# Performance work log

Hardware: AMD Instinct MI355X
Metric: run time of the kernel (lower is better)

Reference implementation:

```python
import jax, jax.numpy as jnp
import numpy as np

H = 2048
MAX_DEPTH = 2
BASIS = 4


def setup_inputs() -> dict:
    key = jax.random.key(0)
    ks = jax.random.split(key, 16)
    s = 0.02

    def w(k, shape):
        return jax.random.normal(k, shape, dtype=jnp.float32) * s

    return dict(
        x=jax.random.normal(ks[0], (1, H), dtype=jnp.float32),
        h=jax.random.normal(ks[1], (1, H), dtype=jnp.float32),
        c=jax.random.normal(ks[2], (1, H), dtype=jnp.float32),
        Wq=w(ks[3], (H, H)), Wk=w(ks[4], (H, H)), Wv=w(ks[5], (H, H)), Wo=w(ks[6], (H, H)),
        Wih=w(ks[7], (H, 4 * H)), Whh=w(ks[8], (H, 4 * H)),
        b_lstm=jnp.zeros((4 * H,), jnp.float32),
        router_w=w(ks[9], (H, BASIS)), router_b=jnp.zeros((BASIS,), jnp.float32),
        expert_w=w(ks[10], (BASIS, H, H)), expert_b=jnp.zeros((BASIS, H), jnp.float32),
        dr_w=w(ks[11], (H, MAX_DEPTH + 1)),
        # bias the depth router toward the deepest choice so the recursion tree is exercised
        dr_b=jnp.array([0.0, 1.0, 5.0], jnp.float32),
        ram_w=w(ks[12], (2 * H, H)), ram_b=jnp.zeros((H,), jnp.float32),
        ag_w=w(ks[13], (2 * H, H)), ag_b=jnp.zeros((H,), jnp.float32),
    )


def reference(x, h, c, Wq, Wk, Wv, Wo, Wih, Whh, b_lstm, router_w, router_b,
              expert_w, expert_b, dr_w, dr_b, ram_w, ram_b, ag_w, ag_b):
    def cell_step(x_, h_, c_):
        # Single-token multi-head attention: softmax over a length-1 axis is
        # identically 1, so attention collapses to (h @ Wv) @ Wo; Wq/Wk are
        # parameters with zero effective gradient (matches torch behavior).
        attn = (h_ @ Wv) @ Wo
        gates = x_ @ Wih + attn @ Whh + b_lstm  # [1, 4H]
        i, f, g, o = jnp.split(gates, 4, axis=1)
        c2 = jax.nn.sigmoid(f) * c_ + jax.nn.sigmoid(i) * jnp.tanh(g)
        h2 = jax.nn.sigmoid(o) * jnp.tanh(c2)
        return h2, h2, c2

    def path_gate(hh):
        p = jax.nn.softmax(hh @ router_w + router_b, axis=1)          # [1, E]
        eo = jnp.einsum('bh,ehk->bek', hh, expert_w) + expert_b        # [1, E, H]
        return jnp.einsum('be,bek->bk', p, eo)                         # [1, H]

    def ramanujan(states):
        # alternating-harmonic (Ramanujan-summation style) weighted reduction
        agg = states[0] * 0.0
        for n, s in enumerate(states):
            agg = agg + (((-1.0) ** n) / (n + 1)) * s
        return jnp.concatenate([agg, states[0]], axis=1) @ ram_w + ram_b

    def fwd(x_, h_, c_, depth):
        so, hs, cs = cell_step(x_, h_, c_)
        hp = path_gate(hs)
        # mirrors torch.no_grad() + .item() host sync
        chosen = int(jnp.argmax(hp @ dr_w + dr_b, axis=1)[0])
        steps = min(chosen, max(0, MAX_DEPTH - depth))
        if steps <= 0:
            return so, hp, cs
        h_cur, c_cur, final = hp, cs, so
        states = [h_cur]
        for _ in range(steps):
            damping = 1.0 / (depth + 1) ** 2
            ro, hnr, cn = fwd(x_, h_cur, c_cur, depth + 1)
            h_next = h_cur + damping * (hnr - h_cur)  # torch.lerp
            states.append(h_next)
            h_cur, c_cur, final = h_next, cn, ro
        anchor = ramanujan(states)
        g = jax.nn.sigmoid(jnp.concatenate([h_cur, anchor], axis=1) @ ag_w + ag_b)
        return final, g * anchor + (1.0 - g) * h_cur, c_cur

    return fwd(x, h, c, 0)
```

## Files before the change

kernel.cpp:

```cpp
#include <hip/hip_runtime.h>
#include <math.h>


#define H 2048
#define NB 512
#define PREP_NB 2048
typedef unsigned short u16;
typedef float f4v __attribute__((ext_vector_type(4)));

struct P {
  const float *x, *h0, *c0, *Wv, *Wo, *Wih, *Whh, *b_lstm, *router_w, *router_b,
              *expert_w, *expert_b, *dr_w, *dr_b, *ram_w, *ram_b, *ag_w, *ag_b;
  const u16 *bWv, *bWo, *bWhh, *bEx, *bRam, *bAg;
  u16 *mWv, *mWo, *mWhh, *mEx, *mRam, *mAg;
  float* out;
  float* ws;
};

constexpr int CTRU   = 16384;
constexpr int DL     = 16384;
constexpr int GT     = 16400;
constexpr int NODE   = 24592;
constexpr int NODESZ = 26624;
constexpr int THV = 0, ATT = 2048, GAC = 4096, EO = 12288, SO = 20480, CS = 22528, HP = 24576;
constexpr int FIN    = NODE + 5 * NODESZ;
constexpr int FINSZ  = 8192;
constexpr int ANC = 0, GCC = 2048, HNo = 4096, AGGo = 6144;
constexpr int RH1 = FIN + 3 * FINSZ;
constexpr int RF1 = RH1 + 2048;
constexpr int RC1 = RH1 + 4096;
constexpr int ZTOT = 5 * 20480 + 3 * 4096;
constexpr size_t BF_BYTE_OFF = 786432;
constexpr size_t oWo  = 4194304;
constexpr size_t oWhh = 8388608;
constexpr size_t oEx  = 25165824;
constexpr size_t oRam = 41943040;
constexpr size_t oAg  = 50331648;
constexpr size_t BF_NODE = 41943040;
constexpr size_t BF_ALL  = 58720256;

__device__ __forceinline__ float sigm(float v) { return 1.f / (1.f + expf(-v)); }

__device__ __forceinline__ float coh_f(const float* p) {
  return __hip_atomic_load(p, __ATOMIC_RELAXED, __HIP_MEMORY_SCOPE_AGENT);
}
__device__ __forceinline__ void coh_st(float* p, float v) {
  __hip_atomic_store(p, v, __ATOMIC_RELAXED, __HIP_MEMORY_SCOPE_AGENT);
}

__device__ __forceinline__ float bfl(unsigned u) { union { unsigned x; float f; } c; c.x = u << 16; return c.f; }
__device__ __forceinline__ float bfh(unsigned u) { union { unsigned x; float f; } c; c.x = u & 0xFFFF0000u; return c.f; }
__device__ __forceinline__ u16 f2bf(float f) {
  unsigned u = __float_as_uint(f);
  u += 0x7FFFu + ((u >> 16) & 1u);
  return (u16)(u >> 16);
}
__device__ __forceinline__ unsigned pk2(float a, float b) {
  return (unsigned)f2bf(a) | ((unsigned)f2bf(b) << 16);
}

template <typename WT> struct W4;
template <> struct W4<float> {
  static __device__ __forceinline__ void load(const float* p, float* w) {
    const float4 v = *reinterpret_cast<const float4*>(p);
    w[0] = v.x; w[1] = v.y; w[2] = v.z; w[3] = v.w;
  }
};
template <> struct W4<u16> {
  static __device__ __forceinline__ void load(const u16* p, float* w) {
    const uint2 u = *reinterpret_cast<const uint2*>(p);
    w[0] = bfl(u.x); w[1] = bfh(u.x); w[2] = bfl(u.y); w[3] = bfh(u.y);
  }
};

template <typename WT> __device__ __forceinline__ const WT* selWv(const P& p);
template <> __device__ __forceinline__ const float* selWv<float>(const P& p) { return p.Wv; }
template <> __device__ __forceinline__ const u16*   selWv<u16>(const P& p)   { return p.bWv; }
template <typename WT> __device__ __forceinline__ const WT* selWo(const P& p);
template <> __device__ __forceinline__ const float* selWo<float>(const P& p) { return p.Wo; }
template <> __device__ __forceinline__ const u16*   selWo<u16>(const P& p)   { return p.bWo; }
template <typename WT> __device__ __forceinline__ const WT* selWhh(const P& p);
template <> __device__ __forceinline__ const float* selWhh<float>(const P& p) { return p.Whh; }
template <> __device__ __forceinline__ const u16*   selWhh<u16>(const P& p)   { return p.bWhh; }
template <typename WT> __device__ __forceinline__ const WT* selEx(const P& p);
template <> __device__ __forceinline__ const float* selEx<float>(const P& p) { return p.expert_w; }
template <> __device__ __forceinline__ const u16*   selEx<u16>(const P& p)   { return p.bEx; }
template <typename WT> __device__ __forceinline__ const WT* selRam(const P& p);
template <> __device__ __forceinline__ const float* selRam<float>(const P& p) { return p.ram_w; }
template <> __device__ __forceinline__ const u16*   selRam<u16>(const P& p)   { return p.bRam; }
template <typename WT> __device__ __forceinline__ const WT* selAg(const P& p);
template <> __device__ __forceinline__ const float* selAg<float>(const P& p) { return p.ag_w; }
template <> __device__ __forceinline__ const u16*   selAg<u16>(const P& p)   { return p.bAg; }

__device__ __forceinline__ int dsteps(const float* dla, const float* drb, int mx) {
  const float l0 = coh_f(dla + 0) + drb[0];
  const float l1 = coh_f(dla + 1) + drb[1];
  const float l2 = coh_f(dla + 2) + drb[2];
  int ch = 0; float bv = l0;
  if (l1 > bv) { bv = l1; ch = 1; }
  if (l2 > bv) { bv = l2; ch = 2; }
  return ch < mx ? ch : mx;
}

__device__ __forceinline__ bool pred(const float* ws, const float* drb, int code) {
  if (code == 0) return true;
  const int s0 = dsteps(ws + DL, drb, 2);
  switch (code) {
    case 1: return s0 >= 1;
    case 2: return s0 >= 1 && dsteps(ws + DL + 4, drb, 1) >= 1;
    case 3: return s0 >= 2;
    case 4: return s0 >= 2 && dsteps(ws + DL + 8, drb, 1) >= 1;
  }
  return true;
}

__device__ __forceinline__ void resbar(unsigned* ctr, int phase) {
  asm volatile("s_waitcnt vmcnt(0)" ::: "memory");
  __syncthreads();
  __shared__ int lastB;
  if (threadIdx.x == 0) {
    lastB = 0;
    unsigned* line = ctr + (blockIdx.x & 31) * 16;
    const unsigned prev = __hip_atomic_fetch_add(line, 1u, __ATOMIC_RELAXED, __HIP_MEMORY_SCOPE_AGENT);
    if (prev == (unsigned)(16 * phase) - 1u) {
      const unsigned m = __hip_atomic_fetch_add(ctr + 512, 1u, __ATOMIC_RELAXED, __HIP_MEMORY_SCOPE_AGENT);
      if (m == (unsigned)(32 * phase) - 1u) lastB = 1;
    }
  }
  __syncthreads();
  if (lastB) {
    if (threadIdx.x < 32)
      __hip_atomic_store(ctr + (40 + threadIdx.x) * 16, (unsigned)phase,
                         __ATOMIC_RELAXED, __HIP_MEMORY_SCOPE_AGENT);
  } else if (threadIdx.x == 0) {
    const unsigned* rel = ctr + (40 + (blockIdx.x & 31)) * 16;
    long t = 0;
    while (__hip_atomic_load(rel, __ATOMIC_RELAXED, __HIP_MEMORY_SCOPE_AGENT) < (unsigned)phase) {
      __builtin_amdgcn_s_sleep(2);
      if (++t > 30000000L) break;
    }
  }
  __syncthreads();
}

template <int CHUNK, int XMODE, typename WT, int CONV, int TPB>
__device__ __forceinline__ void gemv_phase(
    int bid, int G,
    const float* xA, const float* xB, int splitPt, const float* xBias,
    const WT* __restrict__ W, float* __restrict__ y, int N,
    u16* convDst, float* shx, float4* red)
{
  constexpr int NSUB = TPB / 64;
  constexpr int LEN  = CHUNK / NSUB;
  const int tid = threadIdx.x, lane = tid & 63, tsub = tid >> 6;
  const int g = bid % G, s = bid / G;
  const int base = s * CHUNK;
  for (int idx = tid; idx < CHUNK; idx += TPB) {
    const int i = base + idx;
    float v;
    if (XMODE == 0)      v = (i < splitPt) ? coh_f(xA + i) : coh_f(xB + (i - splitPt));
    else if (XMODE == 1) v = coh_f(xA + i);
    else                 v = (i < splitPt) ? coh_f(xA + i)
                                           : (xBias[i - splitPt] + coh_f(xB + (i - splitPt)));
    shx[idx] = v;
  }
  __syncthreads();
  const int j = (g << 8) + (lane << 2);
  const WT* Wp = W + (size_t)(base + tsub * LEN) * N + j;
  float ax = 0.f, ay = 0.f, az = 0.f, aw = 0.f;
#pragma unroll
  for (int t = 0; t < LEN; ++t) {
    const float xi = shx[tsub * LEN + t];
    float w[4];
    if constexpr (CONV) {
      const f4v a = __builtin_nontemporal_load(
          reinterpret_cast<const f4v*>(reinterpret_cast<const float*>(Wp) + (size_t)t * N));
      w[0] = a.x; w[1] = a.y; w[2] = a.z; w[3] = a.w;
      uint2 o; o.x = pk2(w[0], w[1]); o.y = pk2(w[2], w[3]);
      *reinterpret_cast<uint2*>(convDst + (size_t)(base + tsub * LEN + t) * N + j) = o;
    } else {
      W4<WT>::load(Wp + (size_t)t * N, w);
    }
    ax = fmaf(xi, w[0], ax); ay = fmaf(xi, w[1], ay);
    az = fmaf(xi, w[2], az); aw = fmaf(xi, w[3], aw);
  }
  red[tid] = make_float4(ax, ay, az, aw);
  __syncthreads();
  if (tsub == 0) {
    float4 a = red[tid];
#pragma unroll
    for (int q = 1; q < NSUB; ++q) {
      const float4 b = red[tid + q * 64];
      a.x += b.x; a.y += b.y; a.z += b.z; a.w += b.w;
    }
    atomicAdd(&y[j + 0], a.x);
    atomicAdd(&y[j + 1], a.y);
    atomicAdd(&y[j + 2], a.z);
    atomicAdd(&y[j + 3], a.w);
  }
}

template <typename WT, int CONV>
__device__ void expert_phase(const P& p, float* nb, const float* c_in, const float* gt,
                             u16* convDst, float* shx, float4* red)
{
  const int tid = threadIdx.x, lane = tid & 63, w = tid >> 6;
  const int g = blockIdx.x & 31, s = blockIdx.x >> 5;
  const int i0 = s * 128;
  if (tid < 128) {
    const int i = i0 + tid;
    const float gi = p.b_lstm[i]         + coh_f(gt + i)         + coh_f(nb + GAC + i);
    const float gf = p.b_lstm[H + i]     + coh_f(gt + H + i)     + coh_f(nb + GAC + H + i);
    const float gg = p.b_lstm[2 * H + i] + coh_f(gt + 2 * H + i) + coh_f(nb + GAC + 2 * H + i);
    const float go = p.b_lstm[3 * H + i] + coh_f(gt + 3 * H + i) + coh_f(nb + GAC + 3 * H + i);
    const float c2 = sigm(gf) * coh_f(c_in + i) + sigm(gi) * tanhf(gg);
    const float h2 = sigm(go) * tanhf(c2);
    shx[tid] = h2;
    if (g == 0) { coh_st(nb + SO + i, h2); coh_st(nb + CS + i, c2); }
  }
  __syncthreads();
  const int j = (g << 8) + (lane << 2);
  const int e = j >> 11, k = j & (H - 1);
  const size_t tileOff = ((size_t)e << 22) + (size_t)(i0 + w * 16) * H + k;
  const WT* Wp = selEx<WT>(p) + tileOff;
  float ax = 0.f, ay = 0.f, az = 0.f, aw = 0.f;
#pragma unroll
  for (int t = 0; t < 16; ++t) {
    const float xi = shx[w * 16 + t];
    float wv[4];
    if constexpr (CONV) {
      const f4v a = __builtin_nontemporal_load(
          reinterpret_cast<const f4v*>(reinterpret_cast<const float*>(Wp) + (size_t)t * H));
      wv[0] = a.x; wv[1] = a.y; wv[2] = a.z; wv[3] = a.w;
      uint2 o; o.x = pk2(wv[0], wv[1]); o.y = pk2(wv[2], wv[3]);
      *reinterpret_cast<uint2*>(convDst + tileOff + (size_t)t * H) = o;
    } else {
      W4<WT>::load(Wp + (size_t)t * H, wv);
    }
    ax = fmaf(xi, wv[0], ax); ay = fmaf(xi, wv[1], ay);
    az = fmaf(xi, wv[2], az); aw = fmaf(xi, wv[3], aw);
  }
  red[tid] = make_float4(ax, ay, az, aw);
  __syncthreads();
  if (w == 0) {
    float4 a = red[tid];
#pragma unroll
    for (int q = 1; q < 8; ++q) {
      const float4 b = red[tid + q * 64];
      a.x += b.x; a.y += b.y; a.z += b.z; a.w += b.w;
    }
    atomicAdd(&nb[EO + j + 0], a.x);
    atomicAdd(&nb[EO + j + 1], a.y);
    atomicAdd(&nb[EO + j + 2], a.z);
    atomicAdd(&nb[EO + j + 3], a.w);
  }
}

template <typename WT, int CONV>
__device__ __forceinline__ void node_body(const P& p, float* nb,
                                          const float* hv, const float* cv,
                                          unsigned* ctr, int& ph,
                                          float* shx, float4* red)
{
  gemv_phase<32, 1, WT, CONV, 512>(blockIdx.x, 8, hv, nullptr, 0, nullptr,
                                   selWv<WT>(p), nb + THV, H, p.mWv, shx, red);
  resbar(ctr, ++ph);
  gemv_phase<32, 1, WT, CONV, 512>(blockIdx.x, 8, nb + THV, nullptr, 0, nullptr,
                                   selWo<WT>(p), nb + ATT, H, p.mWo, shx, red);
  resbar(ctr, ++ph);
  gemv_phase<128, 1, WT, CONV, 512>(blockIdx.x, 32, nb + ATT, nullptr, 0, nullptr,
                                    selWhh<WT>(p), nb + GAC, 4 * H, p.mWhh, shx, red);
  resbar(ctr, ++ph);
  expert_phase<WT, CONV>(p, nb, cv, p.ws + GT, p.mEx, shx, red);
  resbar(ctr, ++ph);
}

template <typename WT, int CONV>
__device__ __forceinline__ void fin_body(const P& p, float* fb,
                                         const float* aggv, const float* phpv, const float* hnv,
                                         unsigned* ctr, int& ph,
                                         float* shx, float4* red)
{
  gemv_phase<64, 0, WT, CONV, 512>(blockIdx.x, 8, aggv, phpv, H, nullptr,
                                   selRam<WT>(p), fb + ANC, H, p.mRam, shx, red);
  resbar(ctr, ++ph);
  gemv_phase<64, 2, WT, CONV, 512>(blockIdx.x, 8, hnv, fb + ANC, H, p.ram_b,
                                   selAg<WT>(p), fb + GCC, H, p.mAg, shx, red);
  resbar(ctr, ++ph);
}

__device__ void combine_phase(const P& p, float* nb, float* dla, int leaf, float damping,
                              const float* php, float* hn, float* agg, float4* red)
{
  const int tid = threadIdx.x;
  float r0 = 0.f, r1 = 0.f, r2 = 0.f, r3 = 0.f;
  for (int i = tid; i < H; i += 512) {
    const float hh = coh_f(nb + SO + i);
    const float4 rw = *reinterpret_cast<const float4*>(p.router_w + i * 4);
    r0 = fmaf(hh, rw.x, r0); r1 = fmaf(hh, rw.y, r1);
    r2 = fmaf(hh, rw.z, r2); r3 = fmaf(hh, rw.w, r3);
  }
  red[tid] = make_float4(r0, r1, r2, r3);
  __syncthreads();
  for (int off = 256; off > 0; off >>= 1) {
    if (tid < off) {
      const float4 b = red[tid + off];
      red[tid].x += b.x; red[tid].y += b.y; red[tid].z += b.z; red[tid].w += b.w;
    }
    __syncthreads();
  }
  const float4 L = red[0];
  __syncthreads();
  const float l0 = L.x + p.router_b[0], l1 = L.y + p.router_b[1];
  const float l2 = L.z + p.router_b[2], l3 = L.w + p.router_b[3];
  const float m = fmaxf(fmaxf(l0, l1), fmaxf(l2, l3));
  const float e0 = expf(l0 - m), e1 = expf(l1 - m), e2 = expf(l2 - m), e3 = expf(l3 - m);
  const float inv = 1.f / (e0 + e1 + e2 + e3);
  const float q0 = e0 * inv, q1 = e1 * inv, q2 = e2 * inv, q3 = e3 * inv;
  const int jj = blockIdx.x * 256 + (tid & 255);
  float v = 0.f;
  if (tid < 256) {
    v = q0 * (p.expert_b[jj]         + coh_f(nb + EO + jj))
      + q1 * (p.expert_b[H + jj]     + coh_f(nb + EO + H + jj))
      + q2 * (p.expert_b[2 * H + jj] + coh_f(nb + EO + 2 * H + jj))
      + q3 * (p.expert_b[3 * H + jj] + coh_f(nb + EO + 3 * H + jj));
  }
  if (leaf) {
    if (tid < 256) {
      const float h0v = coh_f(php + jj);
      const float hnv = h0v + damping * (v - h0v);
      coh_st(hn + jj, hnv);
      coh_st(agg + jj, h0v - 0.5f * hnv);
    }
  } else {
    if (tid < 256) coh_st(nb + HP + jj, v);
    red[tid] = (tid < 256)
        ? make_float4(v * p.dr_w[jj * 3 + 0], v * p.dr_w[jj * 3 + 1], v * p.dr_w[jj * 3 + 2], 0.f)
        : make_float4(0.f, 0.f, 0.f, 0.f);
    __syncthreads();
    for (int off = 256; off > 0; off >>= 1) {
      if (tid < off) {
        const float4 b = red[tid + off];
        red[tid].x += b.x; red[tid].y += b.y; red[tid].z += b.z;
      }
      __syncthreads();
    }
    if (tid == 0) {
      atomicAdd(&dla[0], red[0].x);
      atomicAdd(&dla[1], red[0].y);
      atomicAdd(&dla[2], red[0].z);
    }
  }
}

__device__ void tail_fsel(const P& p, float* ws) {
  if (threadIdx.x >= 256) return;
  if (dsteps(ws + DL, p.dr_b, 2) < 1) return;
  const bool deep = dsteps(ws + DL + 4, p.dr_b, 1) >= 1;
  const int jj = blockIdx.x * 256 + threadIdx.x;
  const float* n1 = ws + NODE + 1 * NODESZ;
  const float* n2 = ws + NODE + 2 * NODESZ;
  const float* fb = ws + FIN;
  float rh, rf, rc;
  if (deep) {
    const float gacc = p.ag_b[jj] + coh_f(fb + GCC + jj);
    const float anc  = p.ram_b[jj] + coh_f(fb + ANC + jj);
    const float g = sigm(gacc);
    rh = g * anc + (1.f - g) * coh_f(fb + HNo + jj);
    rf = coh_f(n2 + SO + jj); rc = coh_f(n2 + CS + jj);
  } else {
    rh = coh_f(n1 + HP + jj); rf = coh_f(n1 + SO + jj); rc = coh_f(n1 + CS + jj);
  }
  coh_st(ws + RH1 + jj, rh); coh_st(ws + RF1 + jj, rf); coh_st(ws + RC1 + jj, rc);
}

__device__ void tail1(const P& p, float* ws) {
  if (threadIdx.x >= 256) return;
  const int s0 = dsteps(ws + DL, p.dr_b, 2);
  if (s0 < 1) return;
  const int jj = blockIdx.x * 256 + threadIdx.x;
  const float* n0 = ws + NODE;
  const float* n3 = ws + NODE + 3 * NODESZ;
  const float* n4 = ws + NODE + 4 * NODESZ;
  const float* fb3 = ws + FIN + FINSZ;
  float* fb0 = ws + FIN + 2 * FINSZ;
  const float r1 = coh_f(ws + RH1 + jj);
  float rh3 = 0.f, rf3 = 0.f, rc3 = 0.f;
  if (s0 >= 2) {
    if (dsteps(ws + DL + 8, p.dr_b, 1) >= 1) {
      const float gacc = p.ag_b[jj] + coh_f(fb3 + GCC + jj);
      const float anc  = p.ram_b[jj] + coh_f(fb3 + ANC + jj);
      const float g = sigm(gacc);
      rh3 = g * anc + (1.f - g) * coh_f(fb3 + HNo + jj);
      rf3 = coh_f(n4 + SO + jj); rc3 = coh_f(n4 + CS + jj);
    } else {
      rh3 = coh_f(n3 + HP + jj); rf3 = coh_f(n3 + SO + jj); rc3 = coh_f(n3 + CS + jj);
    }
  }
  float ag = coh_f(n0 + HP + jj) - 0.5f * r1;
  float hc, oF, oC;
  if (s0 >= 2) { ag += (1.f / 3.f) * rh3; hc = rh3; oF = rf3; oC = rc3; }
  else { hc = r1; oF = coh_f(ws + RF1 + jj); oC = coh_f(ws + RC1 + jj); }
  coh_st(fb0 + AGGo + jj, ag); coh_st(fb0 + HNo + jj, hc);
  p.out[jj] = oF; p.out[2 * H + jj] = oC;
}

__device__ void tail2(const P& p, float* ws) {
  if (threadIdx.x >= 256) return;
  const int s0 = dsteps(ws + DL, p.dr_b, 2);
  const int jj = blockIdx.x * 256 + threadIdx.x;
  const float* n0 = ws + NODE;
  const float* fb0 = ws + FIN + 2 * FINSZ;
  if (s0 == 0) {
    p.out[jj] = coh_f(n0 + SO + jj);
    p.out[H + jj] = coh_f(n0 + HP + jj);
    p.out[2 * H + jj] = coh_f(n0 + CS + jj);
  } else {
    const float gacc = p.ag_b[jj] + coh_f(fb0 + GCC + jj);
    const float anc  = p.ram_b[jj] + coh_f(fb0 + ANC + jj);
    const float g = sigm(gacc);
    p.out[H + jj] = g * anc + (1.f - g) * coh_f(fb0 + HNo + jj);
  }
}

__global__ void __launch_bounds__(256) k_zero(P p) {
  float* ws = p.ws;
  const int gtid = blockIdx.x * 256 + threadIdx.x;
  const int gsz = gridDim.x * 256;
  unsigned* u = (unsigned*)ws;
  for (int i = gtid; i < CTRU; i += gsz) u[i] = 0u;
  if (gtid < 12) ws[DL + gtid] = 0.f;
  for (int i = gtid; i < 8192; i += gsz) ws[GT + i] = 0.f;
}

__global__ void __launch_bounds__(256) k_prep(P p) {
  float* ws = p.ws;
  __shared__ float shx[128];
  __shared__ float4 red[256];
  const size_t gtid = (size_t)blockIdx.x * 256 + threadIdx.x;
  const size_t nthr = (size_t)PREP_NB * 256;
  for (size_t i = gtid; i < (size_t)ZTOT; i += nthr) {
    if (i < 5 * 20480) {
      const int n = (int)(i / 20480), off = (int)(i % 20480);
      ws[NODE + n * NODESZ + off] = 0.f;
    } else {
      const int j = (int)(i - 5 * 20480);
      ws[FIN + (j >> 12) * FINSZ + (j & 4095)] = 0.f;
    }
  }
  gemv_phase<32, 0, float, 0, 256>(blockIdx.x, 32, p.x, p.x, 1 << 30, nullptr,
                                   p.Wih, ws + GT, 4 * H, nullptr, shx, red);
}

template <typename WT, int CONV>
__global__ void __launch_bounds__(512, 2) k_node(
    P p, int nodeIdx, int ctrIdx, int predCode,
    const float* hv, const float* cv, float* dla)
{
  float* ws = p.ws;
  if (!pred(ws, p.dr_b, predCode)) return;
  __shared__ float shx[128];
  __shared__ float4 red[512];
  float* nb = ws + NODE + nodeIdx * NODESZ;
  unsigned* ctr = (unsigned*)ws + ctrIdx * 2048;
  int ph = 0;
  node_body<WT, CONV>(p, nb, hv, cv, ctr, ph, shx, red);
  if (blockIdx.x >= 8) return;
  combine_phase(p, nb, dla, 0, 0.f, nullptr, nullptr, nullptr, red);
}

template <typename WT, typename WTF, int CONVF>
__global__ void __launch_bounds__(512, 2) k_n2fin(P p) {
  float* ws = p.ws;
  if (!pred(ws, p.dr_b, 1)) return;
  __shared__ float shx[128];
  __shared__ float4 red[512];
  float* nb  = ws + NODE + 2 * NODESZ;
  float* n1  = ws + NODE + 1 * NODESZ;
  float* fb1 = ws + FIN;
  unsigned* ctr = (unsigned*)ws + 2 * 2048;
  int ph = 0;
  if (pred(ws, p.dr_b, 2)) {
    node_body<WT, 0>(p, nb, n1 + HP, n1 + CS, ctr, ph, shx, red);
    if (blockIdx.x < 8)
      combine_phase(p, nb, nullptr, 1, 0.25f, n1 + HP, fb1 + HNo, fb1 + AGGo, red);
    resbar(ctr, ++ph);
  }
  fin_body<WTF, CONVF>(p, fb1, fb1 + AGGo, n1 + HP, fb1 + HNo, ctr, ph, shx, red);
  if (blockIdx.x < 8) tail_fsel(p, ws);
}

template <typename WT, typename WTF>
__global__ void __launch_bounds__(512, 2) k_n4fin(P p) {
  float* ws = p.ws;
  __shared__ float shx[128];
  __shared__ float4 red[512];
  float* nb  = ws + NODE + 4 * NODESZ;
  float* n3  = ws + NODE + 3 * NODESZ;
  float* n0  = ws + NODE;
  float* fb3 = ws + FIN + FINSZ;
  float* fb0 = ws + FIN + 2 * FINSZ;
  unsigned* ctr = (unsigned*)ws + 5 * 2048;
  int ph = 0;
  const int s0v = dsteps(ws + DL, p.dr_b, 2);
  if (s0v >= 2 && dsteps(ws + DL + 8, p.dr_b, 1) >= 1) {
    node_body<WT, 0>(p, nb, n3 + HP, n3 + CS, ctr, ph, shx, red);
    if (blockIdx.x < 8)
      combine_phase(p, nb, nullptr, 1, 0.25f, n3 + HP, fb3 + HNo, fb3 + AGGo, red);
    resbar(ctr, ++ph);
    fin_body<WTF, 0>(p, fb3, fb3 + AGGo, n3 + HP, fb3 + HNo, ctr, ph, shx, red);
  }
  if (s0v >= 1) {
    if (blockIdx.x < 8) tail1(p, ws);
    resbar(ctr, ++ph);
    fin_body<WTF, 0>(p, fb0, fb0 + AGGo, n0 + HP, fb0 + HNo, ctr, ph, shx, red);
  }
  if (blockIdx.x < 8) tail2(p, ws);
}

extern "C" void kernel_launch(void* const* d_in, const int* in_sizes, int n_in,
                              void* d_out, int out_size, void* d_ws, size_t ws_size,
                              hipStream_t stream) {
  P p;
  p.x = (const float*)d_in[0];  p.h0 = (const float*)d_in[1];  p.c0 = (const float*)d_in[2];
  p.Wv = (const float*)d_in[5]; p.Wo = (const float*)d_in[6];
  p.Wih = (const float*)d_in[7]; p.Whh = (const float*)d_in[8];
  p.b_lstm = (const float*)d_in[9];
  p.router_w = (const float*)d_in[10]; p.router_b = (const float*)d_in[11];
  p.expert_w = (const float*)d_in[12]; p.expert_b = (const float*)d_in[13];
  p.dr_w = (const float*)d_in[14]; p.dr_b = (const float*)d_in[15];
  p.ram_w = (const float*)d_in[16]; p.ram_b = (const float*)d_in[17];
  p.ag_w = (const float*)d_in[18]; p.ag_b = (const float*)d_in[19];
  p.out = (float*)d_out;
  p.ws = (float*)d_ws;

  const bool useBf    = ws_size >= BF_BYTE_OFF + BF_NODE * 2 + 1024;
  const bool useBfFin = ws_size >= BF_BYTE_OFF + BF_ALL * 2 + 1024;
  u16* bf = (u16*)((char*)d_ws + BF_BYTE_OFF);
  p.bWv = bf;        p.bWo = bf + oWo;   p.bWhh = bf + oWhh;
  p.bEx = bf + oEx;  p.bRam = bf + oRam; p.bAg  = bf + oAg;
  p.mWv = bf;        p.mWo = bf + oWo;   p.mWhh = bf + oWhh;
  p.mEx = bf + oEx;  p.mRam = bf + oRam; p.mAg  = bf + oAg;

  float* ws = p.ws;
  auto nb = [&](int n) { return ws + NODE + n * NODESZ; };

  k_zero<<<16, 256, 0, stream>>>(p);
  k_prep<<<PREP_NB, 256, 0, stream>>>(p);

  if (useBf)
    k_node<float, 1><<<NB, 512, 0, stream>>>(p, 0, 0, 0, p.h0, p.c0, ws + DL);
  else
    k_node<float, 0><<<NB, 512, 0, stream>>>(p, 0, 0, 0, p.h0, p.c0, ws + DL);

  if (useBf)
    k_node<u16, 0><<<NB, 512, 0, stream>>>(p, 1, 1, 1, nb(0) + HP, nb(0) + CS, ws + DL + 4);
  else
    k_node<float, 0><<<NB, 512, 0, stream>>>(p, 1, 1, 1, nb(0) + HP, nb(0) + CS, ws + DL + 4);

  if (useBf && useBfFin)
    k_n2fin<u16, float, 1><<<NB, 512, 0, stream>>>(p);
  else if (useBf)
    k_n2fin<u16, float, 0><<<NB, 512, 0, stream>>>(p);
  else
    k_n2fin<float, float, 0><<<NB, 512, 0, stream>>>(p);

  if (useBf)
    k_node<u16, 0><<<NB, 512, 0, stream>>>(p, 3, 4, 3, ws + RH1, ws + RC1, ws + DL + 8);
  else
    k_node<float, 0><<<NB, 512, 0, stream>>>(p, 3, 4, 3, ws + RH1, ws + RC1, ws + DL + 8);

  if (useBf && useBfFin)
    k_n4fin<u16, u16><<<NB, 512, 0, stream>>>(p);
  else if (useBf)
    k_n4fin<u16, float><<<NB, 512, 0, stream>>>(p);
  else
    k_n4fin<float, float><<<NB, 512, 0, stream>>>(p);
}
```

Measured before the change: 337.6 us.

## Merge node kernels into fewer persistent launches with grid barriers

The seven launches are cut to four. The prep work is folded into k_zero and into the first node kernel, where the x@Wih GEMV runs before a grid barrier. Node 1 is fused with node 2 and fin, and node 3 with node 4 and fin, using resbar barriers between phases. This removes per-launch overhead and gaps between dependent kernels, at the cost of extra in-kernel grid barriers and a tighter reliance on co-residency of all blocks. The counter regions are remapped to match.

```diff
diff --git a/kernel.cpp b/kernel.cpp
--- a/kernel.cpp
+++ b/kernel.cpp
@@ -4,7 +4,6 @@
 
 #define H 2048
 #define NB 512
-#define PREP_NB 2048
 typedef unsigned short u16;
 typedef float f4v __attribute__((ext_vector_type(4)));
 
@@ -102,18 +101,6 @@
   return ch < mx ? ch : mx;
 }
 
-__device__ __forceinline__ bool pred(const float* ws, const float* drb, int code) {
-  if (code == 0) return true;
-  const int s0 = dsteps(ws + DL, drb, 2);
-  switch (code) {
-    case 1: return s0 >= 1;
-    case 2: return s0 >= 1 && dsteps(ws + DL + 4, drb, 1) >= 1;
-    case 3: return s0 >= 2;
-    case 4: return s0 >= 2 && dsteps(ws + DL + 8, drb, 1) >= 1;
-  }
-  return true;
-}
-
 __device__ __forceinline__ void resbar(unsigned* ctr, int phase) {
   asm volatile("s_waitcnt vmcnt(0)" ::: "memory");
   __syncthreads();
@@ -431,84 +418,84 @@
   for (int i = gtid; i < CTRU; i += gsz) u[i] = 0u;
   if (gtid < 12) ws[DL + gtid] = 0.f;
   for (int i = gtid; i < 8192; i += gsz) ws[GT + i] = 0.f;
-}
-
-__global__ void __launch_bounds__(256) k_prep(P p) {
-  float* ws = p.ws;
-  __shared__ float shx[128];
-  __shared__ float4 red[256];
-  const size_t gtid = (size_t)blockIdx.x * 256 + threadIdx.x;
-  const size_t nthr = (size_t)PREP_NB * 256;
-  for (size_t i = gtid; i < (size_t)ZTOT; i += nthr) {
+  for (int i = gtid; i < ZTOT; i += gsz) {
     if (i < 5 * 20480) {
-      const int n = (int)(i / 20480), off = (int)(i % 20480);
+      const int n = i / 20480, off = i % 20480;
       ws[NODE + n * NODESZ + off] = 0.f;
     } else {
-      const int j = (int)(i - 5 * 20480);
+      const int j = i - 5 * 20480;
       ws[FIN + (j >> 12) * FINSZ + (j & 4095)] = 0.f;
     }
   }
-  gemv_phase<32, 0, float, 0, 256>(blockIdx.x, 32, p.x, p.x, 1 << 30, nullptr,
-                                   p.Wih, ws + GT, 4 * H, nullptr, shx, red);
-}
-
-template <typename WT, int CONV>
-__global__ void __launch_bounds__(512, 2) k_node(
-    P p, int nodeIdx, int ctrIdx, int predCode,
-    const float* hv, const float* cv, float* dla)
-{
-  float* ws = p.ws;
-  if (!pred(ws, p.dr_b, predCode)) return;
-  __shared__ float shx[128];
-  __shared__ float4 red[512];
-  float* nb = ws + NODE + nodeIdx * NODESZ;
-  unsigned* ctr = (unsigned*)ws + ctrIdx * 2048;
-  int ph = 0;
-  node_body<WT, CONV>(p, nb, hv, cv, ctr, ph, shx, red);
-  if (blockIdx.x >= 8) return;
-  combine_phase(p, nb, dla, 0, 0.f, nullptr, nullptr, nullptr, red);
-}
-
-template <typename WT, typename WTF, int CONVF>
-__global__ void __launch_bounds__(512, 2) k_n2fin(P p) {
-  float* ws = p.ws;
-  if (!pred(ws, p.dr_b, 1)) return;
-  __shared__ float shx[128];
-  __shared__ float4 red[512];
-  float* nb  = ws + NODE + 2 * NODESZ;
-  float* n1  = ws + NODE + 1 * NODESZ;
-  float* fb1 = ws + FIN;
-  unsigned* ctr = (unsigned*)ws + 2 * 2048;
-  int ph = 0;
-  if (pred(ws, p.dr_b, 2)) {
-    node_body<WT, 0>(p, nb, n1 + HP, n1 + CS, ctr, ph, shx, red);
-    if (blockIdx.x < 8)
-      combine_phase(p, nb, nullptr, 1, 0.25f, n1 + HP, fb1 + HNo, fb1 + AGGo, red);
-    resbar(ctr, ++ph);
-  }
-  fin_body<WTF, CONVF>(p, fb1, fb1 + AGGo, n1 + HP, fb1 + HNo, ctr, ph, shx, red);
-  if (blockIdx.x < 8) tail_fsel(p, ws);
-}
-
-template <typename WT, typename WTF>
-__global__ void __launch_bounds__(512, 2) k_n4fin(P p) {
+}
+
+template <int CONV>
+__global__ void __launch_bounds__(512, 2) k_n0(P p) {
   float* ws = p.ws;
   __shared__ float shx[128];
   __shared__ float4 red[512];
-  float* nb  = ws + NODE + 4 * NODESZ;
+  float* nb = ws + NODE;
+  unsigned* ctr = (unsigned*)ws;
+  int ph = 0;
+  gemv_phase<128, 1, float, 0, 512>(blockIdx.x, 32, p.x, nullptr, 0, nullptr,
+                                    p.Wih, ws + GT, 4 * H, nullptr, shx, red);
+  resbar(ctr, ++ph);
+  node_body<float, CONV>(p, nb, p.h0, p.c0, ctr, ph, shx, red);
+  if (blockIdx.x >= 8) return;
+  combine_phase(p, nb, ws + DL, 0, 0.f, nullptr, nullptr, nullptr, red);
+}
+
+template <typename WT, typename WTF, int CONVF>
+__global__ void __launch_bounds__(512, 2) k_n12fin(P p) {
+  float* ws = p.ws;
+  if (dsteps(ws + DL, p.dr_b, 2) < 1) return;
+  __shared__ float shx[128];
+  __shared__ float4 red[512];
+  float* n1  = ws + NODE + 1 * NODESZ;
+  float* n2  = ws + NODE + 2 * NODESZ;
+  float* n0  = ws + NODE;
+  float* fb1 = ws + FIN;
+  unsigned* ctr = (unsigned*)ws + 1 * 2048;
+  int ph = 0;
+  node_body<WT, 0>(p, n1, n0 + HP, n0 + CS, ctr, ph, shx, red);
+  if (blockIdx.x < 8)
+    combine_phase(p, n1, ws + DL + 4, 0, 0.f, nullptr, nullptr, nullptr, red);
+  resbar(ctr, ++ph);
+  if (dsteps(ws + DL + 4, p.dr_b, 1) >= 1) {
+    node_body<WT, 0>(p, n2, n1 + HP, n1 + CS, ctr, ph, shx, red);
+    if (blockIdx.x < 8)
+      combine_phase(p, n2, nullptr, 1, 0.25f, n1 + HP, fb1 + HNo, fb1 + AGGo, red);
+    resbar(ctr, ++ph);
+  }
+  fin_body<WTF, CONVF>(p, fb1, fb1 + AGGo, n1 + HP, fb1 + HNo, ctr, ph, shx, red);
+  if (blockIdx.x < 8) tail_fsel(p, ws);
+}
+
+template <typename WT, typename WTF>
+__global__ void __launch_bounds__(512, 2) k_n34fin(P p) {
+  float* ws = p.ws;
+  __shared__ float shx[128];
+  __shared__ float4 red[512];
   float* n3  = ws + NODE + 3 * NODESZ;
+  float* n4  = ws + NODE + 4 * NODESZ;
   float* n0  = ws + NODE;
   float* fb3 = ws + FIN + FINSZ;
   float* fb0 = ws + FIN + 2 * FINSZ;
-  unsigned* ctr = (unsigned*)ws + 5 * 2048;
+  unsigned* ctr = (unsigned*)ws + 2 * 2048;
   int ph = 0;
   const int s0v = dsteps(ws + DL, p.dr_b, 2);
-  if (s0v >= 2 && dsteps(ws + DL + 8, p.dr_b, 1) >= 1) {
-    node_body<WT, 0>(p, nb, n3 + HP, n3 + CS, ctr, ph, shx, red);
+  if (s0v >= 2) {
+    node_body<WT, 0>(p, n3, ws + RH1, ws + RC1, ctr, ph, shx, red);
     if (blockIdx.x < 8)
-      combine_phase(p, nb, nullptr, 1, 0.25f, n3 + HP, fb3 + HNo, fb3 + AGGo, red);
+      combine_phase(p, n3, ws + DL + 8, 0, 0.f, nullptr, nullptr, nullptr, red);
     resbar(ctr, ++ph);
-    fin_body<WTF, 0>(p, fb3, fb3 + AGGo, n3 + HP, fb3 + HNo, ctr, ph, shx, red);
+    if (dsteps(ws + DL + 8, p.dr_b, 1) >= 1) {
+      node_body<WT, 0>(p, n4, n3 + HP, n3 + CS, ctr, ph, shx, red);
+      if (blockIdx.x < 8)
+        combine_phase(p, n4, nullptr, 1, 0.25f, n3 + HP, fb3 + HNo, fb3 + AGGo, red);
+      resbar(ctr, ++ph);
+      fin_body<WTF, 0>(p, fb3, fb3 + AGGo, n3 + HP, fb3 + HNo, ctr, ph, shx, red);
+    }
   }
   if (s0v >= 1) {
     if (blockIdx.x < 8) tail1(p, ws);
@@ -542,38 +529,24 @@
   p.mWv = bf;        p.mWo = bf + oWo;   p.mWhh = bf + oWhh;
   p.mEx = bf + oEx;  p.mRam = bf + oRam; p.mAg  = bf + oAg;
 
-  float* ws = p.ws;
-  auto nb = [&](int n) { return ws + NODE + n * NODESZ; };
-
-  k_zero<<<16, 256, 0, stream>>>(p);
-  k_prep<<<PREP_NB, 256, 0, stream>>>(p);
+  k_zero<<<512, 256, 0, stream>>>(p);
 
   if (useBf)
-    k_node<float, 1><<<NB, 512, 0, stream>>>(p, 0, 0, 0, p.h0, p.c0, ws + DL);
+    k_n0<1><<<NB, 512, 0, stream>>>(p);
   else
-    k_node<float, 0><<<NB, 512, 0, stream>>>(p, 0, 0, 0, p.h0, p.c0, ws + DL);
-
-  if (useBf)
-    k_node<u16, 0><<<NB, 512, 0, stream>>>(p, 1, 1, 1, nb(0) + HP, nb(0) + CS, ws + DL + 4);
+    k_n0<0><<<NB, 512, 0, stream>>>(p);
+
+  if (useBf && useBfFin)
+    k_n12fin<u16, float, 1><<<NB, 512, 0, stream>>>(p);
+  else if (useBf)
+    k_n12fin<u16, float, 0><<<NB, 512, 0, stream>>>(p);
   else
-    k_node<float, 0><<<NB, 512, 0, stream>>>(p, 1, 1, 1, nb(0) + HP, nb(0) + CS, ws + DL + 4);
+    k_n12fin<float, float, 0><<<NB, 512, 0, stream>>>(p);
 
   if (useBf && useBfFin)
-    k_n2fin<u16, float, 1><<<NB, 512, 0, stream>>>(p);
+    k_n34fin<u16, u16><<<NB, 512, 0, stream>>>(p);
   else if (useBf)
-    k_n2fin<u16, float, 0><<<NB, 512, 0, stream>>>(p);
+    k_n34fin<u16, float><<<NB, 512, 0, stream>>>(p);
   else
-    k_n2fin<float, float, 0><<<NB, 512, 0, stream>>>(p);
-
-  if (useBf)
-    k_node<u16, 0><<<NB, 512, 0, stream>>>(p, 3, 4, 3, ws + RH1, ws + RC1, ws + DL + 8);
-  else
-    k_node<float, 0><<<NB, 512, 0, stream>>>(p, 3, 4, 3, ws + RH1, ws + RC1, ws + DL + 8);
-
-  if (useBf && useBfFin)
-    k_n4fin<u16, u16><<<NB, 512, 0, stream>>>(p);
-  else if (useBf)
-    k_n4fin<u16, float><<<NB, 512, 0, stream>>>(p);
-  else
-    k_n4fin<float, float><<<NB, 512, 0, stream>>>(p);
-}
+    k_n34fin<float, float><<<NB, 512, 0, stream>>>(p);
+}
```

Result: no change. 332.4 us (-1.5%).
